# Kernel tuning notes

Measured on AMD Instinct MI355X. Metric: run time of the kernel, lower is better.

The kernel has to match this reference:

```python
import jax, jax.numpy as jnp
import numpy as np

# Constants from __init__ (init_kwargs)
BEAM_WIDTH = 3
TEMPERATURE = 1.0
TOP_TOKENS = 5
EPS = np.float32(2.220446049250313e-16)  # sys.float_info.epsilon


def setup_inputs() -> dict:
    key = jax.random.key(0)
    logits = jax.random.normal(key, (8, 512, 32000), dtype=jnp.float32)
    return {"logits": logits}


def reference(logits):
    # Faithful vectorized beam search over (batch, length, vocab) logits.
    # Per original: probs = softmax(logits / T); at every step each of the
    # beam_width beams expands with the SAME per-step distribution's top
    # `top_tokens` tokens, candidate score = beam_score + log(p + eps),
    # then top beam_width candidates are kept (sorted descending).
    B, L, V = logits.shape
    probs = jax.nn.softmax(logits / TEMPERATURE, axis=-1)          # [B,L,V]
    top_vals, top_idx = jax.lax.top_k(probs, TOP_TOKENS)           # [B,L,T]
    logp = jnp.log(top_vals + EPS)                                 # [B,L,T]

    # Beam 0 starts with score 0; others at -inf emulate the single initial
    # beam (valid because TOP_TOKENS >= BEAM_WIDTH, as in the defaults).
    init_scores = jnp.full((B, BEAM_WIDTH), -jnp.inf, dtype=logits.dtype).at[:, 0].set(0.0)
    init_seqs = jnp.zeros((B, BEAM_WIDTH, L), dtype=jnp.int32)

    def step(carry, xs):
        scores, seqs = carry                      # [B,K], [B,K,L]
        lp_t, idx_t, t = xs                       # [B,T], [B,T], scalar
        cand = scores[:, :, None] + lp_t[:, None, :]        # [B,K,T]
        new_scores, flat = jax.lax.top_k(cand.reshape(B, BEAM_WIDTH * TOP_TOKENS), BEAM_WIDTH)
        beam_idx = flat // TOP_TOKENS                        # [B,K] parent beam
        tok_pos = flat % TOP_TOKENS                          # [B,K] which top token
        toks = jnp.take_along_axis(idx_t, tok_pos, axis=1).astype(jnp.int32)  # [B,K]
        seqs = jnp.take_along_axis(seqs, beam_idx[:, :, None], axis=1)        # reorder parents
        seqs = seqs.at[:, :, t].set(toks)
        return (new_scores, seqs), None

    xs = (logp.transpose(1, 0, 2), top_idx.transpose(1, 0, 2), jnp.arange(L))
    (scores, seqs), _ = jax.lax.scan(step, (init_scores, init_seqs), xs)

    tokens = seqs.transpose(0, 2, 1)  # (batch, length, beam_width)
    return tokens, scores             # scores: (batch, beam_width), descending
```

## Files before the change

### kernel.cpp

```cpp
#include <hip/hip_runtime.h>
#include <math.h>


#define NB 8
#define NL 512
#define NV 32000
#define NT 5
#define NK 3
#define NEG_INF (-__builtin_inff())

typedef unsigned long long ull;
typedef float nfloat4 __attribute__((ext_vector_type(4)));

__device__ __forceinline__ ull pack_key(float v, int idx) {
  unsigned u = __float_as_uint(v);
  unsigned m = u ^ ((unsigned)((int)u >> 31) | 0x80000000u);
  return ((ull)m << 32) | (ull)(unsigned)(~idx);
}
__device__ __forceinline__ float key_val(ull k) {
  unsigned m = (unsigned)(k >> 32);
  unsigned u = (m & 0x80000000u) ? (m ^ 0x80000000u) : ~m;
  return __uint_as_float(u);
}
__device__ __forceinline__ int key_idx(ull k) { return (int)~(unsigned)k; }

__device__ __forceinline__ float4 ntload(const float4* p) {
  nfloat4 v = __builtin_nontemporal_load((const nfloat4*)p);
  return make_float4(v.x, v.y, v.z, v.w);
}

__device__ __forceinline__ int compose_map(int f, int g) {
  int h0 = (f >> (2 * (g & 3))) & 3;
  int h1 = (f >> (2 * ((g >> 2) & 3))) & 3;
  int h2 = (f >> (2 * ((g >> 4) & 3))) & 3;
  return h0 | (h1 << 2) | (h2 << 4);
}

__global__ __launch_bounds__(256) void k_rowtop5(const float* __restrict__ logits,
                                                 float* __restrict__ lp_out,
                                                 int* __restrict__ idx_out) {
  __shared__ double wsum[4];
  __shared__ float wtv[4 * 5];
  __shared__ int wti[4 * 5];
  __shared__ float mtv[5];
  __shared__ int mti[5];

  const int row = blockIdx.x;
  const int tid = threadIdx.x;
  const int lane = tid & 63;
  const int wv = tid >> 6;

  const float4* __restrict__ x4 = (const float4*)(logits + (size_t)row * NV);

  ull K0 = 0, K1 = 0, K2 = 0, K3 = 0, K4 = 0;
  double sum = 0.0;

#define INS_KEY(KEY)                                                           \
  {                                                                            \
    ull key_ = (KEY);                                                          \
    bool b0_ = key_ > K0, b1_ = key_ > K1, b2_ = key_ > K2;                    \
    bool b3_ = key_ > K3, b4_ = key_ > K4;                                     \
    K4 = b4_ ? (b3_ ? K3 : key_) : K4;                                         \
    K3 = b3_ ? (b2_ ? K2 : key_) : K3;                                         \
    K2 = b2_ ? (b1_ ? K1 : key_) : K2;                                         \
    K1 = b1_ ? (b0_ ? K0 : key_) : K1;                                         \
    K0 = b0_ ? key_ : K0;                                                      \
  }

  float4 f0 = ntload(&x4[tid]);
  {
    float e01 = __expf(f0.x - 4.0f) + __expf(f0.y - 4.0f);
    float e23 = __expf(f0.z - 4.0f) + __expf(f0.w - 4.0f);
    sum += (double)(e01 + e23);
  }
  {
    ull c0 = pack_key(f0.x, tid * 4 + 0);
    ull c1 = pack_key(f0.y, tid * 4 + 1);
    ull c2 = pack_key(f0.z, tid * 4 + 2);
    ull c3 = pack_key(f0.w, tid * 4 + 3);
#pragma unroll
    for (int r = 0; r < 5; ++r) {
      ull a_ = c0 > c1 ? c0 : c1;
      ull b_ = c2 > c3 ? c2 : c3;
      ull wb = a_ > b_ ? a_ : b_;
#pragma unroll
      for (int d = 1; d < 64; d <<= 1) {
        ull o = __shfl_xor(wb, d);
        wb = o > wb ? o : wb;
      }
      INS_KEY(wb);
      c0 = (c0 == wb) ? 0ULL : c0;
      c1 = (c1 == wb) ? 0ULL : c1;
      c2 = (c2 == wb) ? 0ULL : c2;
      c3 = (c3 == wb) ? 0ULL : c3;
    }
  }
  float tv4f = key_val(K4);

#define SLOW(CVAL, E)                                                          \
  {                                                                            \
    ull mm_ = __ballot((CVAL) >= tv4f);                                        \
    while (mm_) {                                                              \
      int l_ = __ffsll((unsigned long long)mm_) - 1;                           \
      mm_ &= mm_ - 1;                                                          \
      float bv_ = __shfl((CVAL), l_);                                          \
      int bidx_ = (vbase + l_) * 4 + (E);                                      \
      INS_KEY(pack_key(bv_, bidx_));                                           \
    }                                                                          \
  }

#define COMP(Q, KB)                                                            \
  {                                                                            \
    float ex = __expf((Q).x - 4.0f), ey = __expf((Q).y - 4.0f);                \
    float ez = __expf((Q).z - 4.0f), ew = __expf((Q).w - 4.0f);                \
    sum += (double)((ex + ey) + (ez + ew));                                    \
    float m4 = fmaxf(fmaxf((Q).x, (Q).y), fmaxf((Q).z, (Q).w));                \
    if (__ballot(m4 >= tv4f)) {                                                \
      const int vbase = (tid - lane) + 256 * (KB);                             \
      SLOW((Q).x, 0)                                                           \
      SLOW((Q).y, 1)                                                           \
      SLOW((Q).z, 2)                                                           \
      SLOW((Q).w, 3)                                                           \
      tv4f = key_val(K4);                                                      \
    }                                                                          \
  }

#define GLOAD(Q, KB)                                                           \
  {                                                                            \
    int vv = tid + 256 * (KB);                                                 \
    vv = (vv < NV / 4) ? vv : tid;                                             \
    (Q) = ntload(&x4[vv]);                                                     \
  }

  float4 q0, q1, q2, q3;
  GLOAD(q0, 1) GLOAD(q1, 2) GLOAD(q2, 3) GLOAD(q3, 4)
  for (int k = 1; k <= 25; k += 4) {
    COMP(q0, k)     GLOAD(q0, k + 4)
    COMP(q1, k + 1) GLOAD(q1, k + 5)
    COMP(q2, k + 2) GLOAD(q2, k + 6)
    COMP(q3, k + 3) GLOAD(q3, k + 7)
  }
  COMP(q0, 29)
  COMP(q1, 30)
  if (tid < 64) {
    COMP(q2, 31)
  }
#undef GLOAD
#undef COMP
#undef SLOW
#undef INS_KEY

#pragma unroll
  for (int d = 1; d < 64; d <<= 1) sum += __shfl_xor(sum, d);
  if (lane == 0) wsum[wv] = sum;

  if (lane < 5) {
    ull myk = (lane == 0) ? K0 : (lane == 1) ? K1 : (lane == 2) ? K2
            : (lane == 3) ? K3 : K4;
    wtv[wv * 5 + lane] = key_val(myk);
    wti[wv * 5 + lane] = key_idx(myk);
  }
  __syncthreads();

  if (tid == 0) {
    int h0 = 0, h1 = 0, h2 = 0, h3 = 0;
#pragma unroll
    for (int k = 0; k < 5; ++k) {
      float v0 = (h0 < 5) ? wtv[0 + h0] : NEG_INF;  int j0 = (h0 < 5) ? wti[0 + h0] : 0x7fffffff;
      float v1 = (h1 < 5) ? wtv[5 + h1] : NEG_INF;  int j1 = (h1 < 5) ? wti[5 + h1] : 0x7fffffff;
      float v2 = (h2 < 5) ? wtv[10 + h2] : NEG_INF; int j2 = (h2 < 5) ? wti[10 + h2] : 0x7fffffff;
      float v3 = (h3 < 5) ? wtv[15 + h3] : NEG_INF; int j3 = (h3 < 5) ? wti[15 + h3] : 0x7fffffff;
      float bv = v0; int bj = j0; int bs = 0;
      if (v1 > bv || (v1 == bv && j1 < bj)) { bv = v1; bj = j1; bs = 1; }
      if (v2 > bv || (v2 == bv && j2 < bj)) { bv = v2; bj = j2; bs = 2; }
      if (v3 > bv || (v3 == bv && j3 < bj)) { bv = v3; bj = j3; bs = 3; }
      mtv[k] = bv; mti[k] = bj;
      h0 += (bs == 0); h1 += (bs == 1); h2 += (bs == 2); h3 += (bs == 3);
    }
  }
  __syncthreads();

  if (tid < 5) {
    const double S = wsum[0] + wsum[1] + wsum[2] + wsum[3];
    double p = exp((double)mtv[tid] - 4.0) / S;
    float lp = (float)log(p + 2.220446049250313e-16);
    lp_out[row * 5 + tid] = lp;
    idx_out[row * 5 + tid] = mti[tid];
  }
}

__global__ __launch_bounds__(64) void k_beamscan(const float* __restrict__ lp_in,
                                                 const int* __restrict__ idx_in,
                                                 float* __restrict__ out) {
  __shared__ float lpc[(NL + 8) * 3];
  __shared__ int idxL[NL * NT];
  __shared__ unsigned char selb[NL / 4];

  const int b = blockIdx.x;
  const int tid = threadIdx.x;

  const int4* ip = (const int4*)(idx_in + (size_t)b * NL * NT);
  for (int i = tid; i < NL * NT / 4; i += 64) ((int4*)idxL)[i] = ip[i];
  const float* lpb = lp_in + (size_t)b * NL * NT;
  for (int i = tid; i < NL; i += 64) {
    lpc[i * 3 + 0] = lpb[i * 5 + 0];
    lpc[i * 3 + 1] = lpb[i * 5 + 1];
    lpc[i * 3 + 2] = lpb[i * 5 + 2];
  }
  if (tid < 24) lpc[NL * 3 + tid] = 0.f;
  __syncthreads();

  if (tid == 0) {
    float s0 = 0.f, s1 = NEG_INF, s2 = NEG_INF;
    float lA0 = lpc[0], lA1 = lpc[1],  lA2 = lpc[2];
    float lB0 = lpc[3], lB1 = lpc[4],  lB2 = lpc[5];
    float lC0 = lpc[6], lC1 = lpc[7],  lC2 = lpc[8];
    float lD0 = lpc[9], lD1 = lpc[10], lD2 = lpc[11];
    for (int t = 0; t < NL; t += 4) {
      unsigned byte_ = 0;
      int pfb = (t + 4) * 3;
#define STEP(L0, L1, L2, SH, PF)                                               \
      {                                                                        \
        float c00 = s0 + L0, c01 = s0 + L1, c02 = s0 + L2;                     \
        float c10 = s1 + L0, c20 = s2 + L0;                                    \
        bool a_ = c01 >= c10;                                                  \
        float xv = a_ ? c02 : c01;                                             \
        float yv = a_ ? c10 : c20;                                             \
        bool sb_ = xv >= yv;                                                   \
        s0 = c00;                                                              \
        s1 = a_ ? c01 : c10;                                                   \
        s2 = sb_ ? xv : yv;                                                    \
        byte_ |= ((unsigned)a_ | ((unsigned)sb_ << 1)) << (SH);                \
        PF                                                                     \
      }
      STEP(lA0, lA1, lA2, 0, { lA0 = lpc[pfb + 0]; lA1 = lpc[pfb + 1];  lA2 = lpc[pfb + 2]; })
      STEP(lB0, lB1, lB2, 2, { lB0 = lpc[pfb + 3]; lB1 = lpc[pfb + 4];  lB2 = lpc[pfb + 5]; })
      STEP(lC0, lC1, lC2, 4, { lC0 = lpc[pfb + 6]; lC1 = lpc[pfb + 7];  lC2 = lpc[pfb + 8]; })
      STEP(lD0, lD1, lD2, 6, { lD0 = lpc[pfb + 9]; lD1 = lpc[pfb + 10]; lD2 = lpc[pfb + 11]; })
#undef STEP
      selb[t >> 2] = (unsigned char)byte_;
    }
    out[NB * NL * NK + b * NK + 0] = s0;
    out[NB * NL * NK + b * NK + 1] = s1;
    out[NB * NL * NK + b * NK + 2] = s2;
  }
  __syncthreads();

  const int base = tid * 8;
  unsigned bits0 = selb[(base >> 2) + 0];
  unsigned bits1 = selb[(base >> 2) + 1];
  int e0[8], e1[8], e2[8];
#pragma unroll
  for (int k = 0; k < 8; ++k) {
    int t = base + k;
    unsigned bb = ((k < 4) ? (bits0 >> (2 * k)) : (bits1 >> (2 * (k - 4)))) & 3u;
    int a_ = bb & 1, sb_ = (bb >> 1) & 1;
    int q1 = a_ ? 1 : 0, p1 = a_ ? 0 : 1;
    int q2 = a_ ? (sb_ ? 2 : 0) : (sb_ ? 1 : 0);
    int p2 = a_ ? (sb_ ? 0 : 1) : (sb_ ? 0 : 2);
    e0[k] = idxL[t * NT + 0];
    e1[k] = idxL[t * NT + q1] | (p1 << 20);
    e2[k] = idxL[t * NT + q2] | (p2 << 20);
  }

  const int ID3 = 0 | (1 << 2) | (2 << 4);
  int P = ID3;
#pragma unroll
  for (int k = 7; k >= 0; --k) {
    int g = (e0[k] >> 20) | ((e1[k] >> 20) << 2) | ((e2[k] >> 20) << 4);
    P = compose_map(g, P);
  }
  int X = P;
#pragma unroll
  for (int d = 1; d < 64; d <<= 1) {
    int o = __shfl_down(X, d);
    if (tid + d < 64) X = compose_map(X, o);
  }
  int E = __shfl_down(X, 1);
  if (tid == 63) E = ID3;

  int R = E;
  const int ob = b * NL * NK;
#pragma unroll
  for (int k = 7; k >= 0; --k) {
    int t = base + k;
    int m0 = R & 3, m1 = (R >> 2) & 3, m2 = (R >> 4) & 3;
    int tok0 = (m0 == 0 ? e0[k] : m0 == 1 ? e1[k] : e2[k]) & 0xFFFFF;
    int tok1 = (m1 == 0 ? e0[k] : m1 == 1 ? e1[k] : e2[k]) & 0xFFFFF;
    int tok2 = (m2 == 0 ? e0[k] : m2 == 1 ? e1[k] : e2[k]) & 0xFFFFF;
    out[ob + t * 3 + 0] = (float)tok0;
    out[ob + t * 3 + 1] = (float)tok1;
    out[ob + t * 3 + 2] = (float)tok2;
    int g = (e0[k] >> 20) | ((e1[k] >> 20) << 2) | ((e2[k] >> 20) << 4);
    R = compose_map(g, R);
  }
}

extern "C" void kernel_launch(void* const* d_in, const int* in_sizes, int n_in,
                              void* d_out, int out_size, void* d_ws, size_t ws_size,
                              hipStream_t stream) {
  const float* logits = (const float*)d_in[0];
  float* lp = (float*)d_ws;
  int* idx = (int*)((char*)d_ws + (size_t)NB * NL * NT * sizeof(float));
  float* out = (float*)d_out;

  hipLaunchKernelGGL(k_rowtop5, dim3(NB * NL), dim3(256), 0, stream, logits, lp, idx);
  hipLaunchKernelGGL(k_beamscan, dim3(NB), dim3(64), 0, stream, lp, idx, out);
}
```

Baseline: 121.6 us.

## Widen row top-5 kernel to 1024 threads with wave-shuffle merge

Each row of the logits is now processed by 1024 threads (16 waves) instead of 256, so each thread handles about 8 float4 loads instead of 31. The cross-wave top-5 merge changes from a serial single-thread 4-way merge to a shuffle-based max reduction over 16 wave candidate lists. This cuts the per-block serial chain and load depth per thread. In exchange it adds more blocks' worth of sync and reduction overhead, lowers the number of resident blocks per CU, and shrinks per-thread memory-level parallelism.

```diff
diff --git a/kernel.cpp b/kernel.cpp
--- a/kernel.cpp
+++ b/kernel.cpp
@@ -36,12 +36,12 @@
   return h0 | (h1 << 2) | (h2 << 4);
 }
 
-__global__ __launch_bounds__(256) void k_rowtop5(const float* __restrict__ logits,
-                                                 float* __restrict__ lp_out,
-                                                 int* __restrict__ idx_out) {
-  __shared__ double wsum[4];
-  __shared__ float wtv[4 * 5];
-  __shared__ int wti[4 * 5];
+__global__ __launch_bounds__(1024) void k_rowtop5(const float* __restrict__ logits,
+                                                  float* __restrict__ lp_out,
+                                                  int* __restrict__ idx_out) {
+  __shared__ double wsum[16];
+  __shared__ float wtv[16 * 5];
+  __shared__ int wti[16 * 5];
   __shared__ float mtv[5];
   __shared__ int mti[5];
 
@@ -116,7 +116,7 @@
     sum += (double)((ex + ey) + (ez + ew));                                    \
     float m4 = fmaxf(fmaxf((Q).x, (Q).y), fmaxf((Q).z, (Q).w));                \
     if (__ballot(m4 >= tv4f)) {                                                \
-      const int vbase = (tid - lane) + 256 * (KB);                             \
+      const int vbase = (tid - lane) + 1024 * (KB);                            \
       SLOW((Q).x, 0)                                                           \
       SLOW((Q).y, 1)                                                           \
       SLOW((Q).z, 2)                                                           \
@@ -127,23 +127,21 @@
 
 #define GLOAD(Q, KB)                                                           \
   {                                                                            \
-    int vv = tid + 256 * (KB);                                                 \
+    int vv = tid + 1024 * (KB);                                                \
     vv = (vv < NV / 4) ? vv : tid;                                             \
     (Q) = ntload(&x4[vv]);                                                     \
   }
 
   float4 q0, q1, q2, q3;
   GLOAD(q0, 1) GLOAD(q1, 2) GLOAD(q2, 3) GLOAD(q3, 4)
-  for (int k = 1; k <= 25; k += 4) {
-    COMP(q0, k)     GLOAD(q0, k + 4)
-    COMP(q1, k + 1) GLOAD(q1, k + 5)
-    COMP(q2, k + 2) GLOAD(q2, k + 6)
-    COMP(q3, k + 3) GLOAD(q3, k + 7)
-  }
-  COMP(q0, 29)
-  COMP(q1, 30)
-  if (tid < 64) {
-    COMP(q2, 31)
+  COMP(q0, 1) GLOAD(q0, 5)
+  COMP(q1, 2) GLOAD(q1, 6)
+  COMP(q2, 3) GLOAD(q2, 7)
+  COMP(q3, 4)
+  COMP(q0, 5)
+  COMP(q1, 6)
+  if (tid < 832) {
+    COMP(q2, 7)
   }
 #undef GLOAD
 #undef COMP
@@ -162,26 +160,30 @@
   }
   __syncthreads();
 
-  if (tid == 0) {
-    int h0 = 0, h1 = 0, h2 = 0, h3 = 0;
-#pragma unroll
-    for (int k = 0; k < 5; ++k) {
-      float v0 = (h0 < 5) ? wtv[0 + h0] : NEG_INF;  int j0 = (h0 < 5) ? wti[0 + h0] : 0x7fffffff;
-      float v1 = (h1 < 5) ? wtv[5 + h1] : NEG_INF;  int j1 = (h1 < 5) ? wti[5 + h1] : 0x7fffffff;
-      float v2 = (h2 < 5) ? wtv[10 + h2] : NEG_INF; int j2 = (h2 < 5) ? wti[10 + h2] : 0x7fffffff;
-      float v3 = (h3 < 5) ? wtv[15 + h3] : NEG_INF; int j3 = (h3 < 5) ? wti[15 + h3] : 0x7fffffff;
-      float bv = v0; int bj = j0; int bs = 0;
-      if (v1 > bv || (v1 == bv && j1 < bj)) { bv = v1; bj = j1; bs = 1; }
-      if (v2 > bv || (v2 == bv && j2 < bj)) { bv = v2; bj = j2; bs = 2; }
-      if (v3 > bv || (v3 == bv && j3 < bj)) { bv = v3; bj = j3; bs = 3; }
-      mtv[k] = bv; mti[k] = bj;
-      h0 += (bs == 0); h1 += (bs == 1); h2 += (bs == 2); h3 += (bs == 3);
+  if (wv == 0) {
+    int head = 0;
+#pragma unroll
+    for (int r = 0; r < 5; ++r) {
+      ull hk = 0;
+      if (lane < 16 && head < 5) {
+        hk = pack_key(wtv[lane * 5 + head], wti[lane * 5 + head]);
+      }
+      ull mx = hk;
+#pragma unroll
+      for (int d = 1; d < 64; d <<= 1) {
+        ull o = __shfl_xor(mx, d);
+        mx = o > mx ? o : mx;
+      }
+      if (hk == mx) head++;
+      if (lane == 0) { mtv[r] = key_val(mx); mti[r] = key_idx(mx); }
     }
   }
   __syncthreads();
 
   if (tid < 5) {
-    const double S = wsum[0] + wsum[1] + wsum[2] + wsum[3];
+    double S = wsum[0];
+#pragma unroll
+    for (int i = 1; i < 16; ++i) S += wsum[i];
     double p = exp((double)mtv[tid] - 4.0) / S;
     float lp = (float)log(p + 2.220446049250313e-16);
     lp_out[row * 5 + tid] = lp;
@@ -304,6 +306,6 @@
   int* idx = (int*)((char*)d_ws + (size_t)NB * NL * NT * sizeof(float));
   float* out = (float*)d_out;
 
-  hipLaunchKernelGGL(k_rowtop5, dim3(NB * NL), dim3(256), 0, stream, logits, lp, idx);
+  hipLaunchKernelGGL(k_rowtop5, dim3(NB * NL), dim3(1024), 0, stream, logits, lp, idx);
   hipLaunchKernelGGL(k_beamscan, dim3(NB), dim3(64), 0, stream, lp, idx, out);
 }
```

After: 153.8 us. 1.27x slower.
